# Kernel optimization log

Hardware: AMD Instinct MI355X
Metric: run time of the kernel (lower is better)

## Reference

```python
import jax, jax.numpy as jnp
import numpy as np

L, B, H, R = 128, 4, 768, 24
LN_EPS = 1e-5


def setup_inputs() -> dict:
    key = jax.random.key(0)
    ks = jax.random.split(key, 10)
    s = 1.0 / np.sqrt(H)
    return {
        "h_re": jax.random.normal(ks[0], (L, B, H), jnp.float32),
        "h_share": jax.random.normal(ks[1], (L, B, H), jnp.float32),
        "mask": jnp.ones((L, B), jnp.float32),
        # r: Linear(2H -> H)
        "r_w": jax.random.normal(ks[2], (H, 2 * H), jnp.float32) * s,
        "r_b": jnp.zeros((H,), jnp.float32),
        # hid2hid: Linear(3H -> H)
        "hid_w": jax.random.normal(ks[3], (H, 3 * H), jnp.float32) * s,
        "hid_b": jnp.zeros((H,), jnp.float32),
        # LayerNorm(H)
        "ln_g": jnp.ones((H,), jnp.float32),
        "ln_b": jnp.zeros((H,), jnp.float32),
        # hid2rel: Linear(H -> R)
        "rel_w": jax.random.normal(ks[4], (R, H), jnp.float32) * s,
        "rel_b": jnp.zeros((R,), jnp.float32),
    }


def reference(h_re, h_share, mask, r_w, r_b, hid_w, hid_b, ln_g, ln_b, rel_w, rel_b):
    # h_global = max_over_length( tanh( Linear([h_share; h_re]) ) )  -> [B, H]
    # Decompose concat-linear into two additive projections (same math).
    w_sh, w_re = r_w[:, :H], r_w[:, H:]
    g = jnp.tanh(jnp.einsum('lbh,kh->lbk', h_share, w_sh)
                 + jnp.einsum('lbh,kh->lbk', h_re, w_re) + r_b)
    g = jnp.max(g, axis=0)  # [B, H]

    # hid2hid(cat(r1, r2, g)) = h_re@W1^T (bcast over j) + h_re@W2^T (bcast over i) + g@W3^T + b
    w1, w2, w3 = hid_w[:, :H], hid_w[:, H:2 * H], hid_w[:, 2 * H:]
    p1 = jnp.einsum('lbh,kh->lbk', h_re, w1)        # [L, B, H] -> varies with i
    p2 = jnp.einsum('lbh,kh->lbk', h_re, w2)        # [L, B, H] -> varies with j
    pg = jnp.einsum('bh,kh->bk', g, w3) + hid_b     # [B, H]
    z = p1[:, None, :, :] + p2[None, :, :, :] + pg  # [L, L, B, H]

    # LayerNorm over last dim
    mu = jnp.mean(z, axis=-1, keepdims=True)
    var = jnp.mean(jnp.square(z - mu), axis=-1, keepdims=True)
    z = (z - mu) * jax.lax.rsqrt(var + LN_EPS) * ln_g + ln_b

    # ELU (dropout = identity in eval), then sigmoid(hid2rel)
    z = jax.nn.elu(z)
    re = jax.nn.sigmoid(jnp.einsum('ijbh,rh->ijbr', z, rel_w) + rel_b)  # [L, L, B, R]

    # pairwise mask: mask[i,b] * mask[j,b]
    m = mask[:, None, :] * mask[None, :, :]        # [L, L, B]
    return re * m[..., None]
```

## Files before the change

### kernel.cpp

```cpp
#include <hip/hip_runtime.h>
#include <hip/hip_bf16.h>
#include <math.h>

#define L 128
#define B 4
#define H 768
#define LN_EPS 1e-5f
#define XROWS 272

typedef __attribute__((ext_vector_type(8))) short short8;
typedef __attribute__((ext_vector_type(4))) float f32x4;
typedef __attribute__((ext_vector_type(16))) float f32x16;

static __device__ __forceinline__ unsigned f2bfu(float f) {
    unsigned u = __float_as_uint(f);
    return (u + 0x7FFFu + ((u >> 16) & 1u)) >> 16;
}
static __device__ __forceinline__ uint2 pk4(float4 v) {
    uint2 o;
    o.x = f2bfu(v.x) | (f2bfu(v.y) << 16);
    o.y = f2bfu(v.z) | (f2bfu(v.w) << 16);
    return o;
}
static __device__ __forceinline__ unsigned short f2b(float f) {
    union { __hip_bfloat16 h; unsigned short u; } cv;
    cv.h = __float2bfloat16(f);
    return cv.u;
}
static __device__ __forceinline__ float4 unpk4(uint2 p) {
    return make_float4(__uint_as_float(p.x << 16),
                       __uint_as_float(p.x & 0xffff0000u),
                       __uint_as_float(p.y << 16),
                       __uint_as_float(p.y & 0xffff0000u));
}
static __device__ __forceinline__ unsigned fkey(float x) {
    unsigned u = __float_as_uint(x);
    return (u >> 31) ? ~u : (u | 0x80000000u);
}

__global__ __launch_bounds__(256) void kConv(const float* __restrict__ h_re,
                                             const float* __restrict__ h_share,
                                             const float* __restrict__ r_w,
                                             const float* __restrict__ hid_w,
                                             const float* __restrict__ rel_w,
                                             unsigned short* __restrict__ apack,
                                             unsigned short* __restrict__ wpackA,
                                             unsigned short* __restrict__ wpackB,
                                             unsigned short* __restrict__ rwb2,
                                             unsigned int* __restrict__ gmax) {
    int t = blockIdx.x * 256 + threadIdx.x;
    if (t >= 397056) return;
    if (t < 98304) {
        int m = t / 192, oct = t % 192, k = oct * 8;
        const float* src = (k < 768) ? (h_share + (size_t)m * 768 + k)
                                     : (h_re + (size_t)m * 768 + k - 768);
        float4 x = *(const float4*)src, y = *(const float4*)(src + 4);
        int mt = m >> 4, lr = m & 15, ks = k >> 5, lq = (k >> 3) & 3;
        uint2* dst = (uint2*)(apack + (((size_t)mt * 48 + ks) * 64 + lq * 16 + lr) * 8);
        dst[0] = pk4(x); dst[1] = pk4(y);
    } else if (t < 245760) {
        int t2 = t - 98304;
        int n = t2 / 192, oct = t2 % 192, k = oct * 8;
        const float* src = r_w + (size_t)n * 1536 + k;
        float4 x = *(const float4*)src, y = *(const float4*)(src + 4);
        int nt = n >> 4, lr = n & 15, ks = k >> 5, lq = (k >> 3) & 3;
        uint2* dst = (uint2*)(wpackA + (((size_t)nt * 48 + ks) * 64 + lq * 16 + lr) * 8);
        dst[0] = pk4(x); dst[1] = pk4(y);
    } else if (t < 393216) {
        int t3 = t - 245760;
        int n = t3 / 96, oct = t3 % 96, k = oct * 8;
        int half = (n >= 768) ? 1 : 0;
        const float* src = hid_w + (size_t)(n - half * 768) * 2304 + half * 768 + k;
        float4 x = *(const float4*)src, y = *(const float4*)(src + 4);
        int nt = n >> 4, lr = n & 15, ks = k >> 5, lq = (k >> 3) & 3;
        uint2* dst = (uint2*)(wpackB + (((size_t)nt * 24 + ks) * 64 + lq * 16 + lr) * 8);
        dst[0] = pk4(x); dst[1] = pk4(y);
    } else if (t < 396288) {
        int t4 = t - 393216;
        int s = t4 >> 6, l = t4 & 63;
        int row = l & 31;
        uint2 o0 = make_uint2(0u, 0u), o1 = o0;
        if (row < 24) {
            const float* src = rel_w + (size_t)row * 768 + s * 16 + (l >> 5) * 8;
            o0 = pk4(*(const float4*)src);
            o1 = pk4(*(const float4*)(src + 4));
        }
        uint2* dst = (uint2*)(rwb2 + (size_t)t4 * 8);
        dst[0] = o0; dst[1] = o1;
    } else {
        int t6 = t - 396288;
        gmax[t6] = 0u;
        gmax[768 + t6] = 0u;
        gmax[1536 + t6] = 0u;
        gmax[2304 + t6] = 0u;
    }
}

template<int KSW>
static __device__ __forceinline__ void gemm_steps(const unsigned short* __restrict__ a0p,
                                                  const unsigned short* __restrict__ a1p,
                                                  const unsigned short* __restrict__ w0p,
                                                  const unsigned short* __restrict__ w1p,
                                                  f32x4 acc[2][2]) {
#pragma unroll
    for (int s = 0; s < KSW; s++) {
        short8 a0 = *(const short8*)(a0p + (size_t)s * 512);
        short8 a1 = *(const short8*)(a1p + (size_t)s * 512);
        short8 w0 = *(const short8*)(w0p + (size_t)s * 512);
        short8 w1 = *(const short8*)(w1p + (size_t)s * 512);
        acc[0][0] = __builtin_amdgcn_mfma_f32_16x16x32_bf16(a0, w0, acc[0][0], 0, 0, 0);
        acc[0][1] = __builtin_amdgcn_mfma_f32_16x16x32_bf16(a0, w1, acc[0][1], 0, 0, 0);
        acc[1][0] = __builtin_amdgcn_mfma_f32_16x16x32_bf16(a1, w0, acc[1][0], 0, 0, 0);
        acc[1][1] = __builtin_amdgcn_mfma_f32_16x16x32_bf16(a1, w1, acc[1][1], 0, 0, 0);
    }
}

__global__ __launch_bounds__(256) void kGemm(const unsigned short* __restrict__ apack,
                                             const unsigned short* __restrict__ wpackA,
                                             const unsigned short* __restrict__ wpackB,
                                             unsigned int* __restrict__ gmax,
                                             unsigned short* __restrict__ xb16) {
    __shared__ float red[4][4][64][4];
    int id = blockIdx.x;
    int tid = threadIdx.x, lane = tid & 63, wv = tid >> 6;
    int lq = lane >> 4, lr = lane & 15;
    bool isA = id < 384;
    f32x4 acc[2][2] = {{{0.f,0.f,0.f,0.f},{0.f,0.f,0.f,0.f}},
                       {{0.f,0.f,0.f,0.f},{0.f,0.f,0.f,0.f}}};
    int mt0, nt0;
    if (isA) {
        mt0 = (id / 24) * 2; nt0 = (id % 24) * 2;
        const unsigned short* a0p = apack + ((size_t)mt0 * 48 + wv * 12) * 512 + lane * 8;
        const unsigned short* w0p = wpackA + ((size_t)nt0 * 48 + wv * 12) * 512 + lane * 8;
        gemm_steps<12>(a0p, a0p + 48 * 512, w0p, w0p + 48 * 512, acc);
    } else {
        int id2 = id - 384;
        mt0 = (id2 / 48) * 2; nt0 = (id2 % 48) * 2;
        const unsigned short* a0p = apack + ((size_t)mt0 * 48 + 24 + wv * 6) * 512 + lane * 8;
        const unsigned short* w0p = wpackB + ((size_t)nt0 * 24 + wv * 6) * 512 + lane * 8;
        gemm_steps<6>(a0p, a0p + 48 * 512, w0p, w0p + 24 * 512, acc);
    }
#pragma unroll
    for (int mi = 0; mi < 2; mi++)
#pragma unroll
        for (int ni = 0; ni < 2; ni++)
            *(f32x4*)&red[wv][mi * 2 + ni][lane][0] = acc[mi][ni];
    __syncthreads();
    if (wv != 0) return;

    f32x4 s2[2][2];
#pragma unroll
    for (int mi = 0; mi < 2; mi++)
#pragma unroll
        for (int ni = 0; ni < 2; ni++) {
            f32x4 v = *(f32x4*)&red[0][mi * 2 + ni][lane][0];
#pragma unroll
            for (int w = 1; w < 4; w++) {
                f32x4 u = *(f32x4*)&red[w][mi * 2 + ni][lane][0];
                v[0] += u[0]; v[1] += u[1]; v[2] += u[2]; v[3] += u[3];
            }
            s2[mi][ni] = v;
        }

    if (isA) {
#pragma unroll
        for (int ni = 0; ni < 2; ni++)
#pragma unroll
            for (int q = 0; q < 4; q++) {
                float mx = fmaxf(s2[0][ni][q], s2[1][ni][q]);
                mx = fmaxf(mx, __shfl_xor(mx, 16, 64));
                mx = fmaxf(mx, __shfl_xor(mx, 32, 64));
                if (lq == 0) {
                    int n = (nt0 + ni) * 16 + lr;
                    atomicMax(&gmax[q * 768 + n], fkey(mx));
                }
            }
    } else {
#pragma unroll
        for (int mi = 0; mi < 2; mi++)
#pragma unroll
            for (int ni = 0; ni < 2; ni++)
#pragma unroll
                for (int q = 0; q < 4; q++) {
                    int m = (mt0 + mi) * 16 + lq * 4 + q;
                    int n = (nt0 + ni) * 16 + lr;
                    int b = m & 3, l = m >> 2;
                    size_t row = (n < 768) ? (size_t)l : (size_t)(128 + l);
                    int col = (n < 768) ? n : n - 768;
                    xb16[((size_t)b * XROWS + row) * 768 + col] = f2b(s2[mi][ni][q]);
                }
    }
}

__global__ __launch_bounds__(256) void kPg(const unsigned int* __restrict__ gmax,
                                           const float* __restrict__ r_b,
                                           const float* __restrict__ hid_w,
                                           const float* __restrict__ hid_b,
                                           unsigned short* __restrict__ xb16) {
    __shared__ float sg[768];
    __shared__ float sp[4][64];
    int kt = blockIdx.x, b = blockIdx.y, tid = threadIdx.x;
    for (int v = tid; v < 768; v += 256) {
        unsigned key = gmax[b * 768 + v];
        unsigned bits = (key & 0x80000000u) ? (key & 0x7FFFFFFFu) : ~key;
        sg[v] = tanhf(__uint_as_float(bits) + r_b[v]);
    }
    __syncthreads();
    int kk = tid & 63, hc = tid >> 6;
    int k = kt * 64 + kk;
    const float4* w4 = (const float4*)hid_w;
    const float4* g4 = (const float4*)sg;
    float acc = 0.f;
    for (int h = hc * 48; h < hc * 48 + 48; h++) {
        float4 gv = g4[h];
        float4 wv = w4[(size_t)k * 576 + 384 + h];
        acc += gv.x * wv.x + gv.y * wv.y + gv.z * wv.z + gv.w * wv.w;
    }
    sp[hc][kk] = acc;
    __syncthreads();
    if (hc == 0) {
        float pgv = sp[0][kk] + sp[1][kk] + sp[2][kk] + sp[3][kk] + hid_b[k];
        xb16[((size_t)b * XROWS + 256) * 768 + k] = f2b(pgv);
    }
}

__global__ __launch_bounds__(512, 3) void kC(const unsigned short* __restrict__ xb16,
                                             const float* __restrict__ ln_g,
                                             const float* __restrict__ ln_b,
                                             const unsigned short* __restrict__ rwb2,
                                             const float* __restrict__ rel_b,
                                             const float* __restrict__ mask,
                                             float* __restrict__ out) {
    __shared__ __align__(16) unsigned char smem[49920];
    unsigned short (*zls)[780] = (unsigned short (*)[780])smem;
    int i = blockIdx.x, b = blockIdx.y, j0 = blockIdx.z * 32;
    int tid = threadIdx.x, lane = tid & 63, wave = tid >> 6;

    const uint2* ur = (const uint2*)(xb16 + ((size_t)b * XROWS + i) * 768);
    const uint2* pr = (const uint2*)(xb16 + ((size_t)b * XROWS + 256) * 768);
    const float4* lg4 = (const float4*)ln_g;
    const float4* lb4 = (const float4*)ln_b;
    float4 t1[3], gg[3], bb[3];
#pragma unroll
    for (int s = 0; s < 3; s++) {
        int c = lane + 64 * s;
        float4 x = unpk4(ur[c]), y = unpk4(pr[c]);
        t1[s] = make_float4(x.x + y.x, x.y + y.y, x.z + y.z, x.w + y.w);
        gg[s] = lg4[c];
        bb[s] = lb4[c];
    }

#pragma unroll
    for (int jj = 0; jj < 4; jj++) {
        int j = wave * 4 + jj;
        const uint2* vr2 = (const uint2*)(xb16 + ((size_t)b * XROWS + 128 + j0 + j) * 768);
        float4 z[3];
        float s1 = 0.f, s2 = 0.f;
#pragma unroll
        for (int s = 0; s < 3; s++) {
            float4 vv = unpk4(vr2[lane + 64 * s]);
            vv.x += t1[s].x; vv.y += t1[s].y; vv.z += t1[s].z; vv.w += t1[s].w;
            z[s] = vv;
            s1 += vv.x + vv.y + vv.z + vv.w;
            s2 += vv.x * vv.x + vv.y * vv.y + vv.z * vv.z + vv.w * vv.w;
        }
#pragma unroll
        for (int off = 32; off > 0; off >>= 1) {
            s1 += __shfl_xor(s1, off, 64);
            s2 += __shfl_xor(s2, off, 64);
        }
        float mu = s1 * (1.f / 768.f);
        float rs = rsqrtf(s2 * (1.f / 768.f) - mu * mu + LN_EPS);
        uint2* zrow = (uint2*)&zls[j][0];
#pragma unroll
        for (int s = 0; s < 3; s++) {
            float A0 = rs * gg[s].x, A1 = rs * gg[s].y, A2 = rs * gg[s].z, A3 = rs * gg[s].w;
            float C0 = fmaf(-mu, A0, bb[s].x), C1 = fmaf(-mu, A1, bb[s].y);
            float C2 = fmaf(-mu, A2, bb[s].z), C3 = fmaf(-mu, A3, bb[s].w);
            float z0 = fmaf(z[s].x, A0, C0);
            float z1 = fmaf(z[s].y, A1, C1);
            float z2 = fmaf(z[s].z, A2, C2);
            float z3 = fmaf(z[s].w, A3, C3);
            z0 = fmaxf(z0, __expf(fminf(z0, 0.f)) - 1.f);
            z1 = fmaxf(z1, __expf(fminf(z1, 0.f)) - 1.f);
            z2 = fmaxf(z2, __expf(fminf(z2, 0.f)) - 1.f);
            z3 = fmaxf(z3, __expf(fminf(z3, 0.f)) - 1.f);
            uint2 o;
            o.x = (unsigned)f2b(z0) | ((unsigned)f2b(z1) << 16);
            o.y = (unsigned)f2b(z2) | ((unsigned)f2b(z3) << 16);
            zrow[lane + 64 * s] = o;
        }
    }
    __syncthreads();

    int arow = lane & 31, ahi = lane >> 5;
    f32x16 acc = {0.f,0.f,0.f,0.f, 0.f,0.f,0.f,0.f, 0.f,0.f,0.f,0.f, 0.f,0.f,0.f,0.f};
    const unsigned short* bptr = rwb2 + ((size_t)(wave * 6) * 64 + lane) * 8;
#pragma unroll
    for (int st = 0; st < 6; st++) {
        int s = wave * 6 + st;
        short8 a  = *(const short8*)&zls[arow][s * 16 + ahi * 8];
        short8 bf = *(const short8*)(bptr + (size_t)st * 512);
        acc = __builtin_amdgcn_mfma_f32_32x32x16_bf16(a, bf, acc, 0, 0, 0);
    }
    __syncthreads();
    float* pf = (float*)smem;
#pragma unroll
    for (int r = 0; r < 16; r++) {
        int row = (r & 3) + 8 * (r >> 2) + 4 * ahi;
        pf[wave * 1024 + row * 32 + arow] = acc[r];
    }
    __syncthreads();

#pragma unroll
    for (int e0 = 0; e0 < 2; e0++) {
        int e = tid + e0 * 512;
        int row = e >> 5, col = e & 31;
        if (col < 24) {
            float v = 0.f;
#pragma unroll
            for (int w = 0; w < 8; w++) v += pf[w * 1024 + e];
            int jgl = j0 + row;
            float mval = mask[i * 4 + b] * mask[jgl * 4 + b];
            out[((size_t)(i * 128 + jgl) * 4 + b) * 24 + col] =
                mval / (1.f + __expf(-(v + rel_b[col])));
        }
    }
}

extern "C" void kernel_launch(void* const* d_in, const int* in_sizes, int n_in,
                              void* d_out, int out_size, void* d_ws, size_t ws_size,
                              hipStream_t stream) {
    const float* h_re    = (const float*)d_in[0];
    const float* h_share = (const float*)d_in[1];
    const float* mask    = (const float*)d_in[2];
    const float* r_w     = (const float*)d_in[3];
    const float* r_b     = (const float*)d_in[4];
    const float* hid_w   = (const float*)d_in[5];
    const float* hid_b   = (const float*)d_in[6];
    const float* ln_g    = (const float*)d_in[7];
    const float* ln_b    = (const float*)d_in[8];
    const float* rel_w   = (const float*)d_in[9];
    const float* rel_b   = (const float*)d_in[10];
    float* out = (float*)d_out;

    float* ws = (float*)d_ws;
    unsigned short* apack  = (unsigned short*)(ws);
    unsigned short* wpackA = (unsigned short*)(ws + 393216);
    unsigned short* wpackB = (unsigned short*)(ws + 983040);
    unsigned short* xb16   = (unsigned short*)(ws + 1572864);
    unsigned int*   gmax   = (unsigned int*)(ws + 1990656);
    unsigned short* rwb2   = (unsigned short*)(ws + 1993728);

    kConv<<<1552, 256, 0, stream>>>(h_re, h_share, r_w, hid_w, rel_w,
                                    apack, wpackA, wpackB, rwb2, gmax);
    kGemm<<<1152, 256, 0, stream>>>(apack, wpackA, wpackB, gmax, xb16);
    kPg<<<dim3(12, 4), 256, 0, stream>>>(gmax, r_b, hid_w, hid_b, xb16);
    kC<<<dim3(L, B, 4), 512, 0, stream>>>(xb16, ln_g, ln_b, rwb2, rel_b,
                                          mask, out);
}
```

Measured before the change: 73.12 us.

## Pack p2 into MFMA operand layout and compute rel projection directly from registers

The GEMM epilogue now writes the p2 projection into a pre-swizzled MFMA A-operand layout (vpack) instead of plain rows. kC is restructured so each wave owns 16 j-rows: it computes LayerNorm statistics and the ELU output straight into MFMA register fragments and runs 16x16x32 MFMAs against a repacked rel_w. This drops the LDS staging, the cross-wave reduction and the block barriers. The trade is that each wave reads the inputs twice, once for the statistics and once for normalisation, and smaller blocks do more redundant loads of p1, pg and LN params.

```diff
diff --git a/kernel.cpp b/kernel.cpp
--- a/kernel.cpp
+++ b/kernel.cpp
@@ -10,7 +10,6 @@
 
 typedef __attribute__((ext_vector_type(8))) short short8;
 typedef __attribute__((ext_vector_type(4))) float f32x4;
-typedef __attribute__((ext_vector_type(16))) float f32x16;
 
 static __device__ __forceinline__ unsigned f2bfu(float f) {
     unsigned u = __float_as_uint(f);
@@ -26,12 +25,6 @@
     union { __hip_bfloat16 h; unsigned short u; } cv;
     cv.h = __float2bfloat16(f);
     return cv.u;
-}
-static __device__ __forceinline__ float4 unpk4(uint2 p) {
-    return make_float4(__uint_as_float(p.x << 16),
-                       __uint_as_float(p.x & 0xffff0000u),
-                       __uint_as_float(p.y << 16),
-                       __uint_as_float(p.y & 0xffff0000u));
 }
 static __device__ __forceinline__ unsigned fkey(float x) {
     unsigned u = __float_as_uint(x);
@@ -46,7 +39,7 @@
                                              unsigned short* __restrict__ apack,
                                              unsigned short* __restrict__ wpackA,
                                              unsigned short* __restrict__ wpackB,
-                                             unsigned short* __restrict__ rwb2,
+                                             unsigned short* __restrict__ rwb16,
                                              unsigned int* __restrict__ gmax) {
     int t = blockIdx.x * 256 + threadIdx.x;
     if (t >= 397056) return;
@@ -77,15 +70,16 @@
         dst[0] = pk4(x); dst[1] = pk4(y);
     } else if (t < 396288) {
         int t4 = t - 393216;
-        int s = t4 >> 6, l = t4 & 63;
-        int row = l & 31;
+        int nt = t4 / 1536, ks = (t4 / 64) % 24, l = t4 & 63;
+        int row = nt * 16 + (l & 15);
+        int k = ks * 32 + (l >> 4) * 8;
         uint2 o0 = make_uint2(0u, 0u), o1 = o0;
         if (row < 24) {
-            const float* src = rel_w + (size_t)row * 768 + s * 16 + (l >> 5) * 8;
+            const float* src = rel_w + (size_t)row * 768 + k;
             o0 = pk4(*(const float4*)src);
             o1 = pk4(*(const float4*)(src + 4));
         }
-        uint2* dst = (uint2*)(rwb2 + (size_t)t4 * 8);
+        uint2* dst = (uint2*)(rwb16 + (size_t)t4 * 8);
         dst[0] = o0; dst[1] = o1;
     } else {
         int t6 = t - 396288;
@@ -119,7 +113,8 @@
                                              const unsigned short* __restrict__ wpackA,
                                              const unsigned short* __restrict__ wpackB,
                                              unsigned int* __restrict__ gmax,
-                                             unsigned short* __restrict__ xb16) {
+                                             unsigned short* __restrict__ xb16,
+                                             unsigned short* __restrict__ vpack) {
     __shared__ float red[4][4][64][4];
     int id = blockIdx.x;
     int tid = threadIdx.x, lane = tid & 63, wv = tid >> 6;
@@ -185,9 +180,15 @@
                     int m = (mt0 + mi) * 16 + lq * 4 + q;
                     int n = (nt0 + ni) * 16 + lr;
                     int b = m & 3, l = m >> 2;
-                    size_t row = (n < 768) ? (size_t)l : (size_t)(128 + l);
-                    int col = (n < 768) ? n : n - 768;
-                    xb16[((size_t)b * XROWS + row) * 768 + col] = f2b(s2[mi][ni][q]);
+                    unsigned short val = f2b(s2[mi][ni][q]);
+                    if (n < 768) {
+                        xb16[((size_t)b * XROWS + l) * 768 + n] = val;
+                    } else {
+                        int k = n - 768;
+                        size_t dst = ((((size_t)(b * 8 + (l >> 4)) * 24) + (k >> 5)) * 64
+                                      + ((k >> 3) & 3) * 16 + (l & 15)) * 8 + (k & 7);
+                        vpack[dst] = val;
+                    }
                 }
     }
 }
@@ -224,107 +225,90 @@
     }
 }
 
-__global__ __launch_bounds__(512, 3) void kC(const unsigned short* __restrict__ xb16,
-                                             const float* __restrict__ ln_g,
-                                             const float* __restrict__ ln_b,
-                                             const unsigned short* __restrict__ rwb2,
-                                             const float* __restrict__ rel_b,
-                                             const float* __restrict__ mask,
-                                             float* __restrict__ out) {
-    __shared__ __align__(16) unsigned char smem[49920];
-    unsigned short (*zls)[780] = (unsigned short (*)[780])smem;
-    int i = blockIdx.x, b = blockIdx.y, j0 = blockIdx.z * 32;
+__global__ __launch_bounds__(256) void kC(const unsigned short* __restrict__ xb16,
+                                          const unsigned short* __restrict__ vpack,
+                                          const float* __restrict__ ln_g,
+                                          const float* __restrict__ ln_b,
+                                          const unsigned short* __restrict__ rwb16,
+                                          const float* __restrict__ rel_b,
+                                          const float* __restrict__ mask,
+                                          float* __restrict__ out) {
+    int i = blockIdx.x, b = blockIdx.y;
     int tid = threadIdx.x, lane = tid & 63, wave = tid >> 6;
-
-    const uint2* ur = (const uint2*)(xb16 + ((size_t)b * XROWS + i) * 768);
-    const uint2* pr = (const uint2*)(xb16 + ((size_t)b * XROWS + 256) * 768);
-    const float4* lg4 = (const float4*)ln_g;
-    const float4* lb4 = (const float4*)ln_b;
-    float4 t1[3], gg[3], bb[3];
-#pragma unroll
-    for (int s = 0; s < 3; s++) {
-        int c = lane + 64 * s;
-        float4 x = unpk4(ur[c]), y = unpk4(pr[c]);
-        t1[s] = make_float4(x.x + y.x, x.y + y.y, x.z + y.z, x.w + y.w);
-        gg[s] = lg4[c];
-        bb[s] = lb4[c];
-    }
-
-#pragma unroll
-    for (int jj = 0; jj < 4; jj++) {
-        int j = wave * 4 + jj;
-        const uint2* vr2 = (const uint2*)(xb16 + ((size_t)b * XROWS + 128 + j0 + j) * 768);
-        float4 z[3];
-        float s1 = 0.f, s2 = 0.f;
-#pragma unroll
-        for (int s = 0; s < 3; s++) {
-            float4 vv = unpk4(vr2[lane + 64 * s]);
-            vv.x += t1[s].x; vv.y += t1[s].y; vv.z += t1[s].z; vv.w += t1[s].w;
-            z[s] = vv;
-            s1 += vv.x + vv.y + vv.z + vv.w;
-            s2 += vv.x * vv.x + vv.y * vv.y + vv.z * vv.z + vv.w * vv.w;
+    int jg = blockIdx.z * 4 + wave;
+    int lr = lane & 15, lh = lane >> 4;
+
+    const unsigned short* p1r = xb16 + ((size_t)b * XROWS + i) * 768;
+    const unsigned short* pgr = xb16 + ((size_t)b * XROWS + 256) * 768;
+    const unsigned short* vfr = vpack + (((size_t)(b * 8 + jg) * 24) * 64 + (size_t)lane) * 8;
+
+    float s1 = 0.f, s2 = 0.f;
+    for (int s = 0; s < 24; s++) {
+        int k = s * 32 + lh * 8;
+        uint4 vv = *(const uint4*)(vfr + (size_t)s * 512);
+        uint4 uu = *(const uint4*)(p1r + k);
+        uint4 pp = *(const uint4*)(pgr + k);
+        const unsigned* vw = (const unsigned*)&vv;
+        const unsigned* uw = (const unsigned*)&uu;
+        const unsigned* pw = (const unsigned*)&pp;
+#pragma unroll
+        for (int h = 0; h < 4; h++) {
+            float z0 = __uint_as_float(vw[h] << 16) + __uint_as_float(uw[h] << 16)
+                     + __uint_as_float(pw[h] << 16);
+            float z1 = __uint_as_float(vw[h] & 0xffff0000u) + __uint_as_float(uw[h] & 0xffff0000u)
+                     + __uint_as_float(pw[h] & 0xffff0000u);
+            s1 += z0 + z1;
+            s2 = fmaf(z0, z0, fmaf(z1, z1, s2));
         }
-#pragma unroll
-        for (int off = 32; off > 0; off >>= 1) {
-            s1 += __shfl_xor(s1, off, 64);
-            s2 += __shfl_xor(s2, off, 64);
+    }
+    s1 += __shfl_xor(s1, 16, 64); s1 += __shfl_xor(s1, 32, 64);
+    s2 += __shfl_xor(s2, 16, 64); s2 += __shfl_xor(s2, 32, 64);
+    float mu  = s1 * (1.f / 768.f);
+    float rs  = rsqrtf(s2 * (1.f / 768.f) - mu * mu + LN_EPS);
+    float nmr = -mu * rs;
+
+    f32x4 acc0 = {0.f, 0.f, 0.f, 0.f}, acc1 = {0.f, 0.f, 0.f, 0.f};
+    for (int s = 0; s < 24; s++) {
+        int k = s * 32 + lh * 8;
+        uint4 vv = *(const uint4*)(vfr + (size_t)s * 512);
+        uint4 uu = *(const uint4*)(p1r + k);
+        uint4 pp = *(const uint4*)(pgr + k);
+        float4 g0 = *(const float4*)(ln_g + k), g1 = *(const float4*)(ln_g + k + 4);
+        float4 b0 = *(const float4*)(ln_b + k), b1 = *(const float4*)(ln_b + k + 4);
+        const unsigned* vw = (const unsigned*)&vv;
+        const unsigned* uw = (const unsigned*)&uu;
+        const unsigned* pw = (const unsigned*)&pp;
+        float ge[8] = {g0.x, g0.y, g0.z, g0.w, g1.x, g1.y, g1.z, g1.w};
+        float be[8] = {b0.x, b0.y, b0.z, b0.w, b1.x, b1.y, b1.z, b1.w};
+        short8 a;
+#pragma unroll
+        for (int h = 0; h < 4; h++) {
+            float z0 = __uint_as_float(vw[h] << 16) + __uint_as_float(uw[h] << 16)
+                     + __uint_as_float(pw[h] << 16);
+            float z1 = __uint_as_float(vw[h] & 0xffff0000u) + __uint_as_float(uw[h] & 0xffff0000u)
+                     + __uint_as_float(pw[h] & 0xffff0000u);
+            float t0 = fmaf(fmaf(z0, rs, nmr), ge[2 * h], be[2 * h]);
+            float t1 = fmaf(fmaf(z1, rs, nmr), ge[2 * h + 1], be[2 * h + 1]);
+            t0 = fmaxf(t0, __expf(fminf(t0, 0.f)) - 1.f);
+            t1 = fmaxf(t1, __expf(fminf(t1, 0.f)) - 1.f);
+            a[2 * h]     = (short)f2b(t0);
+            a[2 * h + 1] = (short)f2b(t1);
         }
-        float mu = s1 * (1.f / 768.f);
-        float rs = rsqrtf(s2 * (1.f / 768.f) - mu * mu + LN_EPS);
-        uint2* zrow = (uint2*)&zls[j][0];
-#pragma unroll
-        for (int s = 0; s < 3; s++) {
-            float A0 = rs * gg[s].x, A1 = rs * gg[s].y, A2 = rs * gg[s].z, A3 = rs * gg[s].w;
-            float C0 = fmaf(-mu, A0, bb[s].x), C1 = fmaf(-mu, A1, bb[s].y);
-            float C2 = fmaf(-mu, A2, bb[s].z), C3 = fmaf(-mu, A3, bb[s].w);
-            float z0 = fmaf(z[s].x, A0, C0);
-            float z1 = fmaf(z[s].y, A1, C1);
-            float z2 = fmaf(z[s].z, A2, C2);
-            float z3 = fmaf(z[s].w, A3, C3);
-            z0 = fmaxf(z0, __expf(fminf(z0, 0.f)) - 1.f);
-            z1 = fmaxf(z1, __expf(fminf(z1, 0.f)) - 1.f);
-            z2 = fmaxf(z2, __expf(fminf(z2, 0.f)) - 1.f);
-            z3 = fmaxf(z3, __expf(fminf(z3, 0.f)) - 1.f);
-            uint2 o;
-            o.x = (unsigned)f2b(z0) | ((unsigned)f2b(z1) << 16);
-            o.y = (unsigned)f2b(z2) | ((unsigned)f2b(z3) << 16);
-            zrow[lane + 64 * s] = o;
-        }
-    }
-    __syncthreads();
-
-    int arow = lane & 31, ahi = lane >> 5;
-    f32x16 acc = {0.f,0.f,0.f,0.f, 0.f,0.f,0.f,0.f, 0.f,0.f,0.f,0.f, 0.f,0.f,0.f,0.f};
-    const unsigned short* bptr = rwb2 + ((size_t)(wave * 6) * 64 + lane) * 8;
-#pragma unroll
-    for (int st = 0; st < 6; st++) {
-        int s = wave * 6 + st;
-        short8 a  = *(const short8*)&zls[arow][s * 16 + ahi * 8];
-        short8 bf = *(const short8*)(bptr + (size_t)st * 512);
-        acc = __builtin_amdgcn_mfma_f32_32x32x16_bf16(a, bf, acc, 0, 0, 0);
-    }
-    __syncthreads();
-    float* pf = (float*)smem;
-#pragma unroll
-    for (int r = 0; r < 16; r++) {
-        int row = (r & 3) + 8 * (r >> 2) + 4 * ahi;
-        pf[wave * 1024 + row * 32 + arow] = acc[r];
-    }
-    __syncthreads();
-
-#pragma unroll
-    for (int e0 = 0; e0 < 2; e0++) {
-        int e = tid + e0 * 512;
-        int row = e >> 5, col = e & 31;
-        if (col < 24) {
-            float v = 0.f;
-#pragma unroll
-            for (int w = 0; w < 8; w++) v += pf[w * 1024 + e];
-            int jgl = j0 + row;
-            float mval = mask[i * 4 + b] * mask[jgl * 4 + b];
-            out[((size_t)(i * 128 + jgl) * 4 + b) * 24 + col] =
-                mval / (1.f + __expf(-(v + rel_b[col])));
-        }
+        short8 bf0 = *(const short8*)(rwb16 + ((size_t)s * 64 + lane) * 8);
+        short8 bf1 = *(const short8*)(rwb16 + ((size_t)(24 + s) * 64 + lane) * 8);
+        acc0 = __builtin_amdgcn_mfma_f32_16x16x32_bf16(a, bf0, acc0, 0, 0, 0);
+        acc1 = __builtin_amdgcn_mfma_f32_16x16x32_bf16(a, bf1, acc1, 0, 0, 0);
+    }
+
+    float mi_ = mask[i * 4 + b];
+#pragma unroll
+    for (int q = 0; q < 4; q++) {
+        int jglob = jg * 16 + lh * 4 + q;
+        float mval = mi_ * mask[jglob * 4 + b];
+        size_t ob = ((size_t)(i * 128 + jglob) * 4 + b) * 24;
+        out[ob + lr] = mval / (1.f + __expf(-(acc0[q] + rel_b[lr])));
+        if (lr < 8)
+            out[ob + 16 + lr] = mval / (1.f + __expf(-(acc1[q] + rel_b[16 + lr])));
     }
 }
 
@@ -349,13 +333,14 @@
     unsigned short* wpackA = (unsigned short*)(ws + 393216);
     unsigned short* wpackB = (unsigned short*)(ws + 983040);
     unsigned short* xb16   = (unsigned short*)(ws + 1572864);
-    unsigned int*   gmax   = (unsigned int*)(ws + 1990656);
-    unsigned short* rwb2   = (unsigned short*)(ws + 1993728);
+    unsigned short* vpack  = (unsigned short*)(ws + 1990656);
+    unsigned int*   gmax   = (unsigned int*)(ws + 2187264);
+    unsigned short* rwb16  = (unsigned short*)(ws + 2190336);
 
     kConv<<<1552, 256, 0, stream>>>(h_re, h_share, r_w, hid_w, rel_w,
-                                    apack, wpackA, wpackB, rwb2, gmax);
-    kGemm<<<1152, 256, 0, stream>>>(apack, wpackA, wpackB, gmax, xb16);
+                                    apack, wpackA, wpackB, rwb16, gmax);
+    kGemm<<<1152, 256, 0, stream>>>(apack, wpackA, wpackB, gmax, xb16, vpack);
     kPg<<<dim3(12, 4), 256, 0, stream>>>(gmax, r_b, hid_w, hid_b, xb16);
-    kC<<<dim3(L, B, 4), 512, 0, stream>>>(xb16, ln_g, ln_b, rwb2, rel_b,
-                                          mask, out);
-}
+    kC<<<dim3(128, 4, 2), 256, 0, stream>>>(xb16, vpack, ln_g, ln_b, rwb16,
+                                            rel_b, mask, out);
+}
```

After: 72.69 us. Within noise of the previous version (-0.6%).
